# Performance work log

Measured on AMD Instinct MI355X. Metric: run time of the kernel, lower is better.

The kernel has to match this reference:

```python
import jax, jax.numpy as jnp
import numpy as np

B, S, H = 2, 2048, 2048
NH, NKV, D = 32, 8, 64
GROUPS = NH // NKV
SCALE = D ** -0.5


def rotate_half(x):
    x1, x2 = x[..., : D // 2], x[..., D // 2 :]
    return jnp.concatenate((-x2, x1), axis=-1)


def setup_inputs() -> dict:
    key = jax.random.key(0)
    ks = jax.random.split(key, 8)
    x = jax.random.normal(ks[0], (B, S, H), dtype=jnp.float32)
    cos = jax.random.uniform(ks[1], (B, S, D), dtype=jnp.float32)
    sin = jax.random.uniform(ks[2], (B, S, D), dtype=jnp.float32)
    mask = jnp.tril(jnp.ones((S, S), dtype=jnp.int32))[None, None]  # causal (1,1,S,S)
    std = H ** -0.5
    wq = jax.random.normal(ks[3], (NH * D, H), dtype=jnp.float32) * std
    wk = jax.random.normal(ks[4], (NKV * D, H), dtype=jnp.float32) * std
    wv = jax.random.normal(ks[5], (NKV * D, H), dtype=jnp.float32) * std
    wo = jax.random.normal(ks[6], (H, NH * D), dtype=jnp.float32) * std
    return {"x": x, "cos": cos, "sin": sin, "mask": mask,
            "wq": wq, "wk": wk, "wv": wv, "wo": wo}


def reference(x, cos, sin, mask, wq, wk, wv, wo):
    b, s, _ = x.shape
    # projections (Linear: x @ W^T, no bias)
    q = (x @ wq.T).reshape(b, s, NH, D).transpose(0, 2, 1, 3)    # (b, nh, s, d)
    k = (x @ wk.T).reshape(b, s, NKV, D).transpose(0, 2, 1, 3)   # (b, nkv, s, d)
    v = (x @ wv.T).reshape(b, s, NKV, D).transpose(0, 2, 1, 3)
    # RoPE
    c = cos[:, None, :, :]
    sn = sin[:, None, :, :]
    q = q * c + rotate_half(q) * sn
    k = k * c + rotate_half(k) * sn
    # GQA: repeat KV heads
    k = jnp.repeat(k, GROUPS, axis=1)   # (b, nh, s, d)
    v = jnp.repeat(v, GROUPS, axis=1)
    scores = jnp.einsum("bhqd,bhkd->bhqk", q, k) * SCALE
    scores = jnp.where(mask == 0, -jnp.inf, scores)
    weights = jax.nn.softmax(scores, axis=-1)
    out = jnp.einsum("bhqk,bhkd->bhqd", weights, v)
    out = out.transpose(0, 2, 1, 3).reshape(b, s, NH * D)
    return out @ wo.T
```

## Files before the change

kernel.cpp:

```cpp
#include <hip/hip_runtime.h>
#include <hip/hip_bf16.h>
#include <math.h>

typedef __attribute__((ext_vector_type(8))) short bf16x8;
typedef __attribute__((ext_vector_type(4))) float f32x4;

__device__ __forceinline__ float bf2f(ushort u) {
  union { unsigned u; float f; } v; v.u = ((unsigned)u) << 16; return v.f;
}
__device__ __forceinline__ ushort f2bf(float f) {
  union { float f; unsigned u; } v; v.f = f;
  unsigned r = v.u + 0x7FFFu + ((v.u >> 16) & 1u);
  return (ushort)(r >> 16);
}
#if __has_builtin(__builtin_amdgcn_exp2f)
#define EXP2F(x) __builtin_amdgcn_exp2f(x)
#else
#define EXP2F(x) exp2f(x)
#endif
__device__ __forceinline__ void gl_lds16(const ushort* g, ushort* l) {
  __builtin_amdgcn_global_load_lds(
      (const __attribute__((address_space(1))) unsigned int*)g,
      (__attribute__((address_space(3))) unsigned int*)l, 16, 0, 0);
}

static const long XB   = 0;
static const long WQB  = 8388608;
static const long WKB  = 12582912;
static const long WVB  = 13631488;
static const long WOB  = 14680064;
static const long COSB = 18874368;
static const long SINB = 19136512;
static const long QB   = 19398656;
static const long KB   = 27787264;
static const long VTB  = 29884416;

__global__ void cast_all(const void* __restrict__ s0, const void* __restrict__ s1,
                         const void* __restrict__ s2, const void* __restrict__ s3,
                         const void* __restrict__ s4, const void* __restrict__ s5,
                         const void* __restrict__ s6,
                         ushort* __restrict__ d0, ushort* __restrict__ d1,
                         ushort* __restrict__ d2, ushort* __restrict__ d3,
                         ushort* __restrict__ d4, ushort* __restrict__ d5,
                         ushort* __restrict__ d6, int* __restrict__ flag) {
  __shared__ int cnt;
  if (threadIdx.x == 0) cnt = 0;
  __syncthreads();
  const ushort* xu = (const ushort*)s0;
  int local = 0;
  for (int j = 0; j < 32; j++) {
    ushort u = xu[threadIdx.x + j * 256];
    int e = (u >> 7) & 0xFF;
    if (e >= 100 && e <= 142) local++;
  }
  atomicAdd(&cnt, local);
  __syncthreads();
  const bool isbf = (cnt >= 6554);
  if (threadIdx.x == 0 && blockIdx.x == 0) *flag = isbf ? 1 : 0;
  if (isbf) return;
  const long N = 2424832;
  for (long i = (long)blockIdx.x * blockDim.x + threadIdx.x; i < N;
       i += (long)gridDim.x * blockDim.x) {
    const float4* s; ushort* d; long off;
    if      (i < 1048576) { s = (const float4*)s0; d = d0; off = i; }
    else if (i < 1572864) { s = (const float4*)s1; d = d1; off = i - 1048576; }
    else if (i < 1703936) { s = (const float4*)s2; d = d2; off = i - 1572864; }
    else if (i < 1835008) { s = (const float4*)s3; d = d3; off = i - 1703936; }
    else if (i < 2359296) { s = (const float4*)s4; d = d4; off = i - 1835008; }
    else if (i < 2392064) { s = (const float4*)s5; d = d5; off = i - 2359296; }
    else                  { s = (const float4*)s6; d = d6; off = i - 2392064; }
    float4 a = s[2 * off], b = s[2 * off + 1];
    uint4 o;
    o.x = (unsigned)f2bf(a.x) | ((unsigned)f2bf(a.y) << 16);
    o.y = (unsigned)f2bf(a.z) | ((unsigned)f2bf(a.w) << 16);
    o.z = (unsigned)f2bf(b.x) | ((unsigned)f2bf(b.y) << 16);
    o.w = (unsigned)f2bf(b.z) | ((unsigned)f2bf(b.w) << 16);
    ((uint4*)d)[off] = o;
  }
}

__device__ __forceinline__ void gemm_body(
    const ushort* __restrict__ A, const ushort* __restrict__ W, void* __restrict__ C,
    int N, int K, int bm, int bn, bool ofp32, ushort* As, ushort* Ws) {
  const int tid = threadIdx.x;
  const int wave = tid >> 6, lane = tid & 63;
  const int quad = lane >> 4, l15 = lane & 15;
  const int wm = (wave >> 1) * 64, wn = (wave & 1) * 64;
  const int srow = tid >> 2;
  const int sk = (((tid & 3) ^ ((srow >> 1) & 3)) * 8);
  const ushort* Ap = A + (size_t)(bm + srow) * K + sk;
  const ushort* Wp = W + (size_t)(bn + srow) * K + sk;
  ushort* AsW = As + wave * 512;
  ushort* WsW = Ws + wave * 512;
  const int rq8 = (quad ^ ((l15 >> 1) & 3)) * 8;
  f32x4 acc[4][4] = {};
  for (int k0 = 0; k0 < K; k0 += 32) {
    __syncthreads();
    gl_lds16(Ap + k0, AsW);
    gl_lds16(Ap + (size_t)64 * K + k0, AsW + 2048);
    gl_lds16(Wp + k0, WsW);
    gl_lds16(Wp + (size_t)64 * K + k0, WsW + 2048);
    __syncthreads();
    bf16x8 af[4], wf[4];
#pragma unroll
    for (int t = 0; t < 4; t++)
      af[t] = *(const bf16x8*)&As[(wm + t * 16 + l15) * 32 + rq8];
#pragma unroll
    for (int t = 0; t < 4; t++)
      wf[t] = *(const bf16x8*)&Ws[(wn + t * 16 + l15) * 32 + rq8];
#pragma unroll
    for (int mt = 0; mt < 4; mt++)
#pragma unroll
      for (int nt = 0; nt < 4; nt++)
        acc[mt][nt] = __builtin_amdgcn_mfma_f32_16x16x32_bf16(af[mt], wf[nt], acc[mt][nt], 0, 0, 0);
  }
  if (!ofp32) {
    ushort* Cb = (ushort*)C;
#pragma unroll
    for (int mt = 0; mt < 4; mt++)
#pragma unroll
      for (int nt = 0; nt < 4; nt++)
#pragma unroll
        for (int r = 0; r < 4; r++) {
          int row = bm + wm + mt * 16 + quad * 4 + r;
          int col = bn + wn + nt * 16 + l15;
          Cb[(size_t)row * N + col] = f2bf(acc[mt][nt][r]);
        }
  } else {
    float* Cf = (float*)C;
#pragma unroll
    for (int mt = 0; mt < 4; mt++)
#pragma unroll
      for (int nt = 0; nt < 4; nt++)
#pragma unroll
        for (int r = 0; r < 4; r++) {
          int row = bm + wm + mt * 16 + quad * 4 + r;
          int col = bn + wn + nt * 16 + l15;
          Cf[(size_t)row * N + col] = acc[mt][nt][r];
        }
  }
}

__global__ __launch_bounds__(256) void gemm_qkv(
    const ushort* __restrict__ xws, const ushort* __restrict__ xorig,
    const ushort* __restrict__ wqws, const ushort* __restrict__ wqorig,
    const ushort* __restrict__ wkws, const ushort* __restrict__ wkorig,
    const ushort* __restrict__ wvws, const ushort* __restrict__ wvorig,
    ushort* __restrict__ qout, ushort* __restrict__ kout, ushort* __restrict__ vtout,
    const int* __restrict__ flag) {
  __shared__ __align__(16) ushort As[128 * 32];
  __shared__ __align__(16) ushort Ws[128 * 32];
  const bool bf = (*flag != 0);
  const ushort* x = bf ? xorig : xws;
  const int id = blockIdx.x;
  if (id < 512) {
    gemm_body(x, bf ? wqorig : wqws, qout, 2048, 2048, (id >> 4) * 128, (id & 15) * 128, false, As, Ws);
  } else if (id < 640) {
    int t = id - 512;
    gemm_body(x, bf ? wkorig : wkws, kout, 512, 2048, (t >> 2) * 128, (t & 3) * 128, false, As, Ws);
  } else {
    int t = id - 640;
    gemm_body(bf ? wvorig : wvws, x, vtout, 4096, 2048, (t & 3) * 128, (t >> 2) * 128, false, As, Ws);
  }
}

__global__ __launch_bounds__(256) void gemm_bt(
    const ushort* __restrict__ Aws, const ushort* __restrict__ Aorig,
    const ushort* __restrict__ Wws, const ushort* __restrict__ Worig,
    void* __restrict__ C, int N, int K, const int* __restrict__ flag, int outMode) {
  __shared__ __align__(16) ushort As[128 * 32];
  __shared__ __align__(16) ushort Ws[128 * 32];
  const bool bf = (*flag != 0);
  const ushort* A = (bf && Aorig) ? Aorig : Aws;
  const ushort* W = (bf && Worig) ? Worig : Wws;
  bool ofp32 = (outMode == 1) && !bf;
  gemm_body(A, W, C, N, K, blockIdx.y * 128, blockIdx.x * 128, ofp32, As, Ws);
}

__global__ void rope_kernel(ushort* __restrict__ Kb,
                            const ushort* __restrict__ cws, const ushort* __restrict__ corig,
                            const ushort* __restrict__ sws, const ushort* __restrict__ sorig,
                            const int* __restrict__ flag) {
  const ushort* cb = (*flag) ? corig : cws;
  const ushort* sb = (*flag) ? sorig : sws;
  int j = blockIdx.x * 256 + threadIdx.x;
  long row = j >> 5; int rest = j & 31; int c8 = (rest & 3) * 8;
  ushort* base = Kb + row * 512 + (rest >> 2) * 64 + c8;
  uint4 lo4 = *(const uint4*)base;
  uint4 hi4 = *(const uint4*)(base + 32);
  uint4 cl4 = *(const uint4*)(cb + row * 64 + c8);
  uint4 ch4 = *(const uint4*)(cb + row * 64 + c8 + 32);
  uint4 sl4 = *(const uint4*)(sb + row * 64 + c8);
  uint4 sh4 = *(const uint4*)(sb + row * 64 + c8 + 32);
  const ushort* lo = (const ushort*)&lo4; const ushort* hi = (const ushort*)&hi4;
  const ushort* cl = (const ushort*)&cl4; const ushort* ch = (const ushort*)&ch4;
  const ushort* sl = (const ushort*)&sl4; const ushort* sh = (const ushort*)&sh4;
  uint4 olo, ohi;
  ushort* po = (ushort*)&olo; ushort* ph = (ushort*)&ohi;
#pragma unroll
  for (int k = 0; k < 8; k++) {
    float l = bf2f(lo[k]), h = bf2f(hi[k]);
    po[k] = f2bf(l * bf2f(cl[k]) - h * bf2f(sl[k]));
    ph[k] = f2bf(h * bf2f(ch[k]) + l * bf2f(sh[k]));
  }
  *(uint4*)base = olo;
  *(uint4*)(base + 32) = ohi;
}

__global__ __launch_bounds__(512, 4) void attn_kernel(
    const ushort* __restrict__ Qb, const ushort* __restrict__ Kb,
    const ushort* __restrict__ Vt,
    const ushort* __restrict__ cws, const ushort* __restrict__ corig,
    const ushort* __restrict__ sws, const ushort* __restrict__ sorig,
    ushort* __restrict__ Ob, const int* __restrict__ flag) {
  __shared__ __align__(16) ushort Ks[2][4096];
  __shared__ __align__(16) ushort Vs[2][4096];
  __shared__ __align__(16) ushort Ps[128 * 72];
  const int tid = threadIdx.x;
  const int wave = tid >> 6, lane = tid & 63;
  const int quad = lane >> 4, l15 = lane & 15;
  const int id = blockIdx.x;
  const int kvh = id & 7;
  const int b = (id >> 3) & 1;
  const int hsub = (id >> 4) & 3;
  const int h = kvh * 4 + hsub;
  const int t = 15 - (id >> 6);
  const size_t brow = (size_t)b * 2048;
  const ushort* Kg = Kb + brow * 512 + (size_t)kvh * 64;
  const ushort* Vg = Vt + (size_t)(kvh * 64) * 4096 + brow;

  const int prow = wave * 16 + (lane >> 2);
  const int chunk = (((lane & 3) ^ ((prow >> 1) & 3)) * 8);
  const int k_s = prow & 63, k_kc = prow >> 6;
  const int v_d = prow & 63, v_sc = prow >> 6;
  const int ldsW = wave * 512;

  const int q0 = t * 128;
  const int wrow0 = q0 + wave * 16;
  const int blockNt = 2 * t + 2;
  const int myLast = wrow0 >> 6;

  gl_lds16(Kg + (size_t)k_s * 512 + k_kc * 32 + chunk, &Ks[0][ldsW]);
  gl_lds16(Vg + (size_t)v_d * 4096 + v_sc * 32 + chunk, &Vs[0][ldsW]);

  const ushort* cb = (*flag) ? corig : cws;
  const ushort* sp = (*flag) ? sorig : sws;
  const size_t qrow_g = brow + wrow0 + l15;
  bf16x8 qlo = *(const bf16x8*)&Qb[qrow_g * 2048 + h * 64 + quad * 8];
  bf16x8 qhi = *(const bf16x8*)&Qb[qrow_g * 2048 + h * 64 + 32 + quad * 8];
  bf16x8 cl = *(const bf16x8*)&cb[qrow_g * 64 + quad * 8];
  bf16x8 ch = *(const bf16x8*)&cb[qrow_g * 64 + 32 + quad * 8];
  bf16x8 sl = *(const bf16x8*)&sp[qrow_g * 64 + quad * 8];
  bf16x8 sh = *(const bf16x8*)&sp[qrow_g * 64 + 32 + quad * 8];
  bf16x8 qf[2];
  const float scl = 0.18033688011112f;
#pragma unroll
  for (int j = 0; j < 8; j++) {
    float l = bf2f((ushort)qlo[j]), hg = bf2f((ushort)qhi[j]);
    qf[0][j] = (short)f2bf((l * bf2f((ushort)cl[j]) - hg * bf2f((ushort)sl[j])) * scl);
    qf[1][j] = (short)f2bf((hg * bf2f((ushort)ch[j]) + l * bf2f((ushort)sh[j])) * scl);
  }

  const int rq8 = (quad ^ ((l15 >> 1) & 3)) * 8;

  float lsum0 = 0.f, lsum1 = 0.f;
  f32x4 oacc[4] = {};

  __syncthreads();

  for (int nt = 0; nt < blockNt; nt++) {
    const int cur = nt & 1;
    if (nt + 1 < blockNt) {
      const int n1 = (nt + 1) * 64;
      gl_lds16(Kg + (size_t)(n1 + k_s) * 512 + k_kc * 32 + chunk, &Ks[cur ^ 1][ldsW]);
      gl_lds16(Vg + (size_t)v_d * 4096 + n1 + v_sc * 32 + chunk, &Vs[cur ^ 1][ldsW]);
    }
    if (nt <= myLast) {
      const int n0 = nt * 64;
      const ushort* Kc = Ks[cur];
      const ushort* Vc = Vs[cur];
      f32x4 sc[4];
      __builtin_amdgcn_s_setprio(1);
#pragma unroll
      for (int ct = 0; ct < 4; ct++) {
        bf16x8 kf0 = *(const bf16x8*)&Kc[(ct * 16 + l15) * 32 + rq8];
        bf16x8 kf1 = *(const bf16x8*)&Kc[2048 + (ct * 16 + l15) * 32 + rq8];
        f32x4 z = {0.f, 0.f, 0.f, 0.f};
        z = __builtin_amdgcn_mfma_f32_16x16x32_bf16(kf0, qf[0], z, 0, 0, 0);
        z = __builtin_amdgcn_mfma_f32_16x16x32_bf16(kf1, qf[1], z, 0, 0, 0);
        sc[ct] = z;
      }
      __builtin_amdgcn_s_setprio(0);
      if (nt == myLast) {
        const int qrow = wrow0 + l15;
#pragma unroll
        for (int ct = 0; ct < 4; ct++)
#pragma unroll
          for (int r = 0; r < 4; r++)
            if (n0 + ct * 16 + quad * 4 + r > qrow) sc[ct][r] = -INFINITY;
      }
#pragma unroll
      for (int ct = 0; ct < 4; ct++)
#pragma unroll
        for (int k = 0; k < 2; k++) {
          float pv0 = EXP2F(sc[ct][2 * k]     - 23.083120654223f);
          float pv1 = EXP2F(sc[ct][2 * k + 1] - 23.083120654223f);
          lsum0 += pv0;
          lsum1 += pv1;
          __hip_bfloat162 pk = __float22bfloat162_rn(make_float2(pv0, pv1));
          *(__hip_bfloat162*)&Ps[(wave * 16 + l15) * 72 + ct * 16 + quad * 4 + 2 * k] = pk;
        }
      bf16x8 pf0 = *(const bf16x8*)&Ps[(wave * 16 + l15) * 72 + quad * 8];
      bf16x8 pf1 = *(const bf16x8*)&Ps[(wave * 16 + l15) * 72 + 32 + quad * 8];
      __builtin_amdgcn_s_setprio(1);
#pragma unroll
      for (int dt = 0; dt < 4; dt++) {
        bf16x8 vf0 = *(const bf16x8*)&Vc[(dt * 16 + l15) * 32 + rq8];
        bf16x8 vf1 = *(const bf16x8*)&Vc[2048 + (dt * 16 + l15) * 32 + rq8];
        oacc[dt] = __builtin_amdgcn_mfma_f32_16x16x32_bf16(pf0, vf0, oacc[dt], 0, 0, 0);
        oacc[dt] = __builtin_amdgcn_mfma_f32_16x16x32_bf16(pf1, vf1, oacc[dt], 0, 0, 0);
      }
      __builtin_amdgcn_s_setprio(0);
    }
    __syncthreads();
  }
  float l_loc = lsum0 + lsum1;
  l_loc += __shfl_xor(l_loc, 16, 64);
  l_loc += __shfl_xor(l_loc, 32, 64);
  float linv[4];
#pragma unroll
  for (int r = 0; r < 4; r++) linv[r] = 1.f / __shfl(l_loc, quad * 4 + r, 64);
#pragma unroll
  for (int dt = 0; dt < 4; dt++)
#pragma unroll
    for (int r = 0; r < 4; r++) {
      int s = wrow0 + quad * 4 + r;
      Ob[(brow + s) * 2048 + h * 64 + dt * 16 + l15] = f2bf(oacc[dt][r] * linv[r]);
    }
}

extern "C" void kernel_launch(void* const* d_in, const int* in_sizes, int n_in,
                              void* d_out, int out_size, void* d_ws, size_t ws_size,
                              hipStream_t stream) {
  char* wsb = (char*)d_ws;
  int* flag = (int*)wsb;
  ushort* base = (ushort*)(wsb + 256);
  ushort* xb   = base + XB;
  ushort* wqb  = base + WQB;
  ushort* wkb  = base + WKB;
  ushort* wvb  = base + WVB;
  ushort* wob  = base + WOB;
  ushort* cosb = base + COSB;
  ushort* sinb = base + SINB;
  ushort* qb   = base + QB;
  ushort* kb   = base + KB;
  ushort* vtb  = base + VTB;
  ushort* abuf = xb;

  const ushort* xo  = (const ushort*)d_in[0];
  const ushort* co  = (const ushort*)d_in[1];
  const ushort* so  = (const ushort*)d_in[2];
  const ushort* wqo = (const ushort*)d_in[4];
  const ushort* wko = (const ushort*)d_in[5];
  const ushort* wvo = (const ushort*)d_in[6];
  const ushort* woo = (const ushort*)d_in[7];

  cast_all<<<4096, 256, 0, stream>>>(d_in[0], d_in[4], d_in[5], d_in[6], d_in[7],
                                     d_in[1], d_in[2],
                                     xb, wqb, wkb, wvb, wob, cosb, sinb, flag);

  gemm_qkv<<<768, 256, 0, stream>>>(xb, xo, wqb, wqo, wkb, wko, wvb, wvo,
                                    qb, kb, vtb, flag);

  rope_kernel<<<512, 256, 0, stream>>>(kb, cosb, co, sinb, so, flag);

  attn_kernel<<<1024, 512, 0, stream>>>(qb, kb, vtb, cosb, co, sinb, so, abuf, flag);

  gemm_bt<<<dim3(16, 32), 256, 0, stream>>>(abuf, nullptr, wob, woo, d_out, 2048, 2048, flag, 1);
}
```

Before: 306.5 us.

## Use 256x256 double-buffered GEMM tiles with 8 waves for projections

Replaces the 128x128 single-buffered GEMM body with a 256x256 tile computed by 512 threads. Each wave now owns a 128x64 sub-tile, and K tiles are double-buffered in LDS with global_load_lds prefetch two stages ahead, using vmcnt waits and s_setprio around the MFMAs. This raises operand reuse per byte loaded and overlaps loads with compute. The cost is far fewer blocks (192 and 128, against 256 CUs), which leaves many CUs idle and can cause load imbalance. It also raises register pressure from the 8x4 accumulator array.

```diff
diff --git a/kernel.cpp b/kernel.cpp
--- a/kernel.cpp
+++ b/kernel.cpp
@@ -79,102 +79,132 @@
   }
 }
 
-__device__ __forceinline__ void gemm_body(
+__device__ __forceinline__ void gemm256(
     const ushort* __restrict__ A, const ushort* __restrict__ W, void* __restrict__ C,
     int N, int K, int bm, int bn, bool ofp32, ushort* As, ushort* Ws) {
   const int tid = threadIdx.x;
   const int wave = tid >> 6, lane = tid & 63;
   const int quad = lane >> 4, l15 = lane & 15;
-  const int wm = (wave >> 1) * 64, wn = (wave & 1) * 64;
-  const int srow = tid >> 2;
-  const int sk = (((tid & 3) ^ ((srow >> 1) & 3)) * 8);
-  const ushort* Ap = A + (size_t)(bm + srow) * K + sk;
-  const ushort* Wp = W + (size_t)(bn + srow) * K + sk;
-  ushort* AsW = As + wave * 512;
-  ushort* WsW = Ws + wave * 512;
+  const int wm = (wave >> 2) * 128;
+  const int wn = (wave & 3) * 64;
+  const int srow = wave * 16 + (lane >> 2);
+  const int sg8 = (((lane & 3) ^ ((lane >> 3) & 3)) * 8);
   const int rq8 = (quad ^ ((l15 >> 1) & 3)) * 8;
-  f32x4 acc[4][4] = {};
-  for (int k0 = 0; k0 < K; k0 += 32) {
-    __syncthreads();
-    gl_lds16(Ap + k0, AsW);
-    gl_lds16(Ap + (size_t)64 * K + k0, AsW + 2048);
-    gl_lds16(Wp + k0, WsW);
-    gl_lds16(Wp + (size_t)64 * K + k0, WsW + 2048);
-    __syncthreads();
-    bf16x8 af[4], wf[4];
-#pragma unroll
-    for (int t = 0; t < 4; t++)
-      af[t] = *(const bf16x8*)&As[(wm + t * 16 + l15) * 32 + rq8];
-#pragma unroll
-    for (int t = 0; t < 4; t++)
-      wf[t] = *(const bf16x8*)&Ws[(wn + t * 16 + l15) * 32 + rq8];
-#pragma unroll
-    for (int mt = 0; mt < 4; mt++)
-#pragma unroll
-      for (int nt = 0; nt < 4; nt++)
-        acc[mt][nt] = __builtin_amdgcn_mfma_f32_16x16x32_bf16(af[mt], wf[nt], acc[mt][nt], 0, 0, 0);
-  }
+  const int T = K >> 5;
+  f32x4 acc[8][4] = {};
+
+#define STAGE256(t, b)                                                        \
+  do {                                                                        \
+    const int k0_ = (t) * 32;                                                 \
+    ushort* ab_ = As + (b) * 8192;                                            \
+    ushort* wb_ = Ws + (b) * 8192;                                            \
+    gl_lds16(A + (size_t)(bm + srow) * K + k0_ + sg8, ab_ + wave * 512);      \
+    gl_lds16(A + (size_t)(bm + 128 + srow) * K + k0_ + sg8, ab_ + 4096 + wave * 512); \
+    gl_lds16(W + (size_t)(bn + srow) * K + k0_ + sg8, wb_ + wave * 512);      \
+    gl_lds16(W + (size_t)(bn + 128 + srow) * K + k0_ + sg8, wb_ + 4096 + wave * 512); \
+  } while (0)
+
+  STAGE256(0, 0);
+  STAGE256(1, 1);
+  asm volatile("s_waitcnt vmcnt(4)" ::: "memory");
+  __builtin_amdgcn_s_barrier();
+  __builtin_amdgcn_sched_barrier(0);
+
+  for (int t = 0; t < T; ++t) {
+    const int cur = t & 1;
+    const ushort* ab = As + cur * 8192;
+    const ushort* wb = Ws + cur * 8192;
+    bf16x8 wf[4];
+#pragma unroll
+    for (int nf = 0; nf < 4; ++nf)
+      wf[nf] = *(const bf16x8*)&wb[(wn + nf * 16 + l15) * 32 + rq8];
+#pragma unroll
+    for (int mf = 0; mf < 8; ++mf) {
+      bf16x8 af = *(const bf16x8*)&ab[(wm + mf * 16 + l15) * 32 + rq8];
+      __builtin_amdgcn_s_setprio(1);
+#pragma unroll
+      for (int nf = 0; nf < 4; ++nf)
+        acc[mf][nf] = __builtin_amdgcn_mfma_f32_16x16x32_bf16(af, wf[nf], acc[mf][nf], 0, 0, 0);
+      __builtin_amdgcn_s_setprio(0);
+    }
+    if (t + 1 < T) {
+      __builtin_amdgcn_sched_barrier(0);
+      __builtin_amdgcn_s_barrier();
+      __builtin_amdgcn_sched_barrier(0);
+      if (t + 2 < T) {
+        STAGE256(t + 2, cur);
+        asm volatile("s_waitcnt vmcnt(4)" ::: "memory");
+      } else {
+        asm volatile("s_waitcnt vmcnt(0)" ::: "memory");
+      }
+      __builtin_amdgcn_s_barrier();
+      __builtin_amdgcn_sched_barrier(0);
+    }
+  }
+#undef STAGE256
+
   if (!ofp32) {
     ushort* Cb = (ushort*)C;
 #pragma unroll
-    for (int mt = 0; mt < 4; mt++)
-#pragma unroll
-      for (int nt = 0; nt < 4; nt++)
-#pragma unroll
-        for (int r = 0; r < 4; r++) {
-          int row = bm + wm + mt * 16 + quad * 4 + r;
-          int col = bn + wn + nt * 16 + l15;
-          Cb[(size_t)row * N + col] = f2bf(acc[mt][nt][r]);
+    for (int mf = 0; mf < 8; ++mf)
+#pragma unroll
+      for (int nf = 0; nf < 4; ++nf)
+#pragma unroll
+        for (int r = 0; r < 4; ++r) {
+          int row = bm + wm + mf * 16 + quad * 4 + r;
+          int col = bn + wn + nf * 16 + l15;
+          Cb[(size_t)row * N + col] = f2bf(acc[mf][nf][r]);
         }
   } else {
     float* Cf = (float*)C;
 #pragma unroll
-    for (int mt = 0; mt < 4; mt++)
-#pragma unroll
-      for (int nt = 0; nt < 4; nt++)
-#pragma unroll
-        for (int r = 0; r < 4; r++) {
-          int row = bm + wm + mt * 16 + quad * 4 + r;
-          int col = bn + wn + nt * 16 + l15;
-          Cf[(size_t)row * N + col] = acc[mt][nt][r];
+    for (int mf = 0; mf < 8; ++mf)
+#pragma unroll
+      for (int nf = 0; nf < 4; ++nf)
+#pragma unroll
+        for (int r = 0; r < 4; ++r) {
+          int row = bm + wm + mf * 16 + quad * 4 + r;
+          int col = bn + wn + nf * 16 + l15;
+          Cf[(size_t)row * N + col] = acc[mf][nf][r];
         }
   }
 }
 
-__global__ __launch_bounds__(256) void gemm_qkv(
+__global__ __launch_bounds__(512, 2) void gemm_qkv(
     const ushort* __restrict__ xws, const ushort* __restrict__ xorig,
     const ushort* __restrict__ wqws, const ushort* __restrict__ wqorig,
     const ushort* __restrict__ wkws, const ushort* __restrict__ wkorig,
     const ushort* __restrict__ wvws, const ushort* __restrict__ wvorig,
     ushort* __restrict__ qout, ushort* __restrict__ kout, ushort* __restrict__ vtout,
     const int* __restrict__ flag) {
-  __shared__ __align__(16) ushort As[128 * 32];
-  __shared__ __align__(16) ushort Ws[128 * 32];
+  __shared__ __align__(16) ushort As[2 * 8192];
+  __shared__ __align__(16) ushort Ws[2 * 8192];
   const bool bf = (*flag != 0);
   const ushort* x = bf ? xorig : xws;
   const int id = blockIdx.x;
-  if (id < 512) {
-    gemm_body(x, bf ? wqorig : wqws, qout, 2048, 2048, (id >> 4) * 128, (id & 15) * 128, false, As, Ws);
-  } else if (id < 640) {
-    int t = id - 512;
-    gemm_body(x, bf ? wkorig : wkws, kout, 512, 2048, (t >> 2) * 128, (t & 3) * 128, false, As, Ws);
+  if (id < 128) {
+    gemm256(x, bf ? wqorig : wqws, qout, 2048, 2048, (id >> 3) * 256, (id & 7) * 256, false, As, Ws);
+  } else if (id < 160) {
+    int t = id - 128;
+    gemm256(x, bf ? wkorig : wkws, kout, 512, 2048, (t >> 1) * 256, (t & 1) * 256, false, As, Ws);
   } else {
-    int t = id - 640;
-    gemm_body(bf ? wvorig : wvws, x, vtout, 4096, 2048, (t & 3) * 128, (t >> 2) * 128, false, As, Ws);
-  }
-}
-
-__global__ __launch_bounds__(256) void gemm_bt(
+    int t = id - 160;
+    gemm256(bf ? wvorig : wvws, x, vtout, 4096, 2048, (t & 1) * 256, (t >> 1) * 256, false, As, Ws);
+  }
+}
+
+__global__ __launch_bounds__(512, 2) void gemm_bt(
     const ushort* __restrict__ Aws, const ushort* __restrict__ Aorig,
     const ushort* __restrict__ Wws, const ushort* __restrict__ Worig,
     void* __restrict__ C, int N, int K, const int* __restrict__ flag, int outMode) {
-  __shared__ __align__(16) ushort As[128 * 32];
-  __shared__ __align__(16) ushort Ws[128 * 32];
+  __shared__ __align__(16) ushort As[2 * 8192];
+  __shared__ __align__(16) ushort Ws[2 * 8192];
   const bool bf = (*flag != 0);
   const ushort* A = (bf && Aorig) ? Aorig : Aws;
   const ushort* W = (bf && Worig) ? Worig : Wws;
   bool ofp32 = (outMode == 1) && !bf;
-  gemm_body(A, W, C, N, K, blockIdx.y * 128, blockIdx.x * 128, ofp32, As, Ws);
+  const int id = blockIdx.x;
+  gemm256(A, W, C, N, K, (id >> 3) * 256, (id & 7) * 256, ofp32, As, Ws);
 }
 
 __global__ void rope_kernel(ushort* __restrict__ Kb,
@@ -369,12 +399,12 @@
                                      d_in[1], d_in[2],
                                      xb, wqb, wkb, wvb, wob, cosb, sinb, flag);
 
-  gemm_qkv<<<768, 256, 0, stream>>>(xb, xo, wqb, wqo, wkb, wko, wvb, wvo,
+  gemm_qkv<<<192, 512, 0, stream>>>(xb, xo, wqb, wqo, wkb, wko, wvb, wvo,
                                     qb, kb, vtb, flag);
 
   rope_kernel<<<512, 256, 0, stream>>>(kb, cosb, co, sinb, so, flag);
 
   attn_kernel<<<1024, 512, 0, stream>>>(qb, kb, vtb, cosb, co, sinb, so, abuf, flag);
 
-  gemm_bt<<<dim3(16, 32), 256, 0, stream>>>(abuf, nullptr, wob, woo, d_out, 2048, 2048, flag, 1);
-}
+  gemm_bt<<<128, 512, 0, stream>>>(abuf, nullptr, wob, woo, d_out, 2048, 2048, flag, 1);
+}
```

Measured after the change: 357.0 us. 16.5% more time.
